# Performance work log

Measured on AMD Instinct MI355X. Metric: run time of the kernel, lower is better.

The kernel has to match this reference:

```python
import jax, jax.numpy as jnp
import numpy as np

VOCAB = 100000
EDIM = 300
MUS = np.array([-0.9, -0.7, -0.5, -0.3, -0.1, 0.1, 0.3, 0.5, 0.7, 0.9, 1.0], dtype=np.float32)
SIGMAS = np.array([0.1] * 10 + [0.001], dtype=np.float32)


def setup_inputs() -> dict:
    key = jax.random.key(0)
    k1, k2, k3, k4, k5, k6 = jax.random.split(key, 6)
    B, Q, D = 128, 16, 1024
    doctoks = jax.random.randint(k1, (B, D), 0, VOCAB)
    querytoks = jax.random.randint(k2, (B, Q), 0, VOCAB)
    query_idf = jax.random.uniform(k3, (B, Q), dtype=jnp.float32)
    emb_table = jax.random.normal(k4, (VOCAB, EDIM), dtype=jnp.float32) * 0.1
    # pad token 0 -> zero embedding (padding_idx semantics)
    emb_table = emb_table.at[0].set(0.0)
    mus = jnp.asarray(MUS)
    sigmas = jnp.asarray(SIGMAS)
    K = mus.shape[0]
    fc_w = jax.random.normal(k5, (1, K), dtype=jnp.float32) * (1.0 / np.sqrt(K))
    fc_b = jax.random.normal(k6, (1,), dtype=jnp.float32) * 0.01
    return {"doctoks": doctoks, "querytoks": querytoks, "query_idf": query_idf,
            "emb_table": emb_table, "mus": mus, "sigmas": sigmas,
            "fc_w": fc_w, "fc_b": fc_b}


def reference(doctoks, querytoks, query_idf, emb_table, mus, sigmas, fc_w, fc_b):
    eps = 1e-9
    q_emb = emb_table[querytoks]                # [B,Q,E]
    d_emb = emb_table[doctoks]                  # [B,D,E]
    qn = q_emb / (jnp.linalg.norm(q_emb, axis=-1, keepdims=True) + eps)
    dn = d_emb / (jnp.linalg.norm(d_emb, axis=-1, keepdims=True) + eps)
    simmat = jnp.einsum('bqe,bde->bqd', qn, dn)  # cosine sim [B,Q,D]
    # zero out padded positions (token id 0)
    pad_mask = (querytoks != 0)[:, :, None] & (doctoks != 0)[:, None, :]
    simmat = jnp.where(pad_mask, simmat, 0.0)
    # RBF kernel bank broadcast at dim=1: [B,K,Q,D]
    diff = simmat[:, None, :, :] - mus[None, :, None, None]
    kernels = jnp.exp(-0.5 * diff * diff / (sigmas[None, :, None, None] ** 2))
    result = kernels.sum(axis=3)                 # [B,K,Q]
    mask = (simmat.sum(axis=2) != 0.0)[:, None, :]  # [B,1,Q] -> broadcasts over K
    mask = jnp.broadcast_to(mask, result.shape)
    result = jnp.where(mask, jnp.log(result + 1e-6), 0.0)
    result = result.sum(axis=2)                  # [B,K]
    scores = result @ fc_w.T + fc_b              # [B,1]
    return scores
```

## Files before the change

kernel.cpp:

```cpp
#include <hip/hip_runtime.h>

#define EDIM 300
#define NB   128
#define NQ   16
#define ND   1024
#define NK   11
#define BLOCK 128
#define MDOC  4
#define TDOCS 256
#define BLOCKS_PER_B 4
#define NPANEL 10
#define PPITCH 36
#define SIMP 260

#define BARRIER_LGKM() do { \
    asm volatile("s_waitcnt lgkmcnt(0)" ::: "memory"); \
    __builtin_amdgcn_s_barrier(); \
    asm volatile("" ::: "memory"); } while (0)

#define PF_L(j)  pf##j = *(const float4*)(rp##j + pp * 32)
#define PF_LOAD(p) do { const int pp = (p); if (pp < 9 || s < 3) { \
    PF_L(0);  PF_L(1);  PF_L(2);  PF_L(3);  PF_L(4);  PF_L(5);  PF_L(6);  PF_L(7); \
    PF_L(8);  PF_L(9);  PF_L(10); PF_L(11); PF_L(12); PF_L(13); PF_L(14); PF_L(15); } } while (0)

#define PF_S(j)  *(float4*)&panel[(r0 + 16 * (j)) * PPITCH + s * 4] = pf##j
#define PF_WRITE(p) do { if ((p) < 9 || s < 3) { \
    PF_S(0);  PF_S(1);  PF_S(2);  PF_S(3);  PF_S(4);  PF_S(5);  PF_S(6);  PF_S(7); \
    PF_S(8);  PF_S(9);  PF_S(10); PF_S(11); PF_S(12); PF_S(13); PF_S(14); PF_S(15); } } while (0)

__global__ __launch_bounds__(BLOCK, 1) void knrm_main(
    const int*   __restrict__ dtoks,
    const int*   __restrict__ qtoks,
    const float* __restrict__ emb,
    const float* __restrict__ mus,
    const float* __restrict__ sigmas,
    float*       __restrict__ part) {
    __shared__ __align__(16) float qn_s[NQ * EDIM];
    __shared__ __align__(16) float panel[TDOCS * PPITCH];
    __shared__ int   dtok_s[TDOCS];
    __shared__ float rs_s[NQ];
    __shared__ __align__(16) float sim_t[NQ * SIMP];
    __shared__ float red_s[NK * NQ * 8];

    const int blk   = blockIdx.x;
    const int b     = blk >> 2;
    const int dbase = (blk & 3) * TDOCS;
    const int tid   = threadIdx.x;
    const int lane  = tid & 63;
    const int w     = tid >> 6;

    for (int i = tid; i < TDOCS; i += BLOCK) dtok_s[i] = dtoks[b * ND + dbase + i];
    for (int i = tid; i < NQ * (EDIM / 4); i += BLOCK) {
        int q = i / (EDIM / 4), e4 = i - q * (EDIM / 4);
        ((float4*)qn_s)[i] =
            *(const float4*)(emb + (size_t)qtoks[b * NQ + q] * EDIM + e4 * 4);
    }
    __syncthreads();

    const int s  = tid & 7;
    const int r0 = tid >> 3;

    const float* rp0  = emb + (size_t)dtok_s[r0 +   0] * EDIM + s * 4;
    const float* rp1  = emb + (size_t)dtok_s[r0 +  16] * EDIM + s * 4;
    const float* rp2  = emb + (size_t)dtok_s[r0 +  32] * EDIM + s * 4;
    const float* rp3  = emb + (size_t)dtok_s[r0 +  48] * EDIM + s * 4;
    const float* rp4  = emb + (size_t)dtok_s[r0 +  64] * EDIM + s * 4;
    const float* rp5  = emb + (size_t)dtok_s[r0 +  80] * EDIM + s * 4;
    const float* rp6  = emb + (size_t)dtok_s[r0 +  96] * EDIM + s * 4;
    const float* rp7  = emb + (size_t)dtok_s[r0 + 112] * EDIM + s * 4;
    const float* rp8  = emb + (size_t)dtok_s[r0 + 128] * EDIM + s * 4;
    const float* rp9  = emb + (size_t)dtok_s[r0 + 144] * EDIM + s * 4;
    const float* rp10 = emb + (size_t)dtok_s[r0 + 160] * EDIM + s * 4;
    const float* rp11 = emb + (size_t)dtok_s[r0 + 176] * EDIM + s * 4;
    const float* rp12 = emb + (size_t)dtok_s[r0 + 192] * EDIM + s * 4;
    const float* rp13 = emb + (size_t)dtok_s[r0 + 208] * EDIM + s * 4;
    const float* rp14 = emb + (size_t)dtok_s[r0 + 224] * EDIM + s * 4;
    const float* rp15 = emb + (size_t)dtok_s[r0 + 240] * EDIM + s * 4;

    float4 pf0, pf1, pf2, pf3, pf4, pf5, pf6, pf7,
           pf8, pf9, pf10, pf11, pf12, pf13, pf14, pf15;

    PF_LOAD(0);
    {
        int q = tid >> 3, j = tid & 7;
        float ss = 0.f;
        for (int e = j; e < EDIM; e += 8) { float v = qn_s[q * EDIM + e]; ss += v * v; }
        ss += __shfl_xor(ss, 1, 64);
        ss += __shfl_xor(ss, 2, 64);
        ss += __shfl_xor(ss, 4, 64);
        if (j == 0) rs_s[q] = 1.0f / (sqrtf(ss) + 1e-9f);
    }
    __syncthreads();
    for (int i = tid; i < NQ * (EDIM / 4); i += BLOCK) {
        float4 v = ((float4*)qn_s)[i];
        float r = rs_s[i / (EDIM / 4)];
        v.x *= r; v.y *= r; v.z *= r; v.w *= r;
        ((float4*)qn_s)[i] = v;
    }
    PF_WRITE(0);
    PF_LOAD(1);
    BARRIER_LGKM();

    float sims[MDOC][8];
#pragma unroll
    for (int m = 0; m < MDOC; ++m)
#pragma unroll
        for (int qq = 0; qq < 8; ++qq) sims[m][qq] = 0.f;
    float ssq[MDOC] = {0.f, 0.f, 0.f, 0.f};

    for (int p = 0; p < NPANEL; ++p) {
        const int cmax = (p == 9) ? 3 : 8;
        for (int cc = 0; cc < cmax; ++cc) {
            float4 dv[MDOC];
#pragma unroll
            for (int m = 0; m < MDOC; ++m)
                dv[m] = *(const float4*)&panel[(lane + 64 * m) * PPITCH + cc * 4];
#pragma unroll
            for (int m = 0; m < MDOC; ++m)
                ssq[m] += dv[m].x*dv[m].x + dv[m].y*dv[m].y + dv[m].z*dv[m].z + dv[m].w*dv[m].w;
            const float* qb = qn_s + (size_t)w * 8 * EDIM + (p * 8 + cc) * 4;
#pragma unroll
            for (int qq = 0; qq < 8; ++qq) {
                float4 qv = *(const float4*)(qb + qq * EDIM);
#pragma unroll
                for (int m = 0; m < MDOC; ++m) {
                    sims[m][qq] += qv.x*dv[m].x + qv.y*dv[m].y + qv.z*dv[m].z + qv.w*dv[m].w;
                }
            }
        }
        BARRIER_LGKM();
        if (p < 9) {
            PF_WRITE(p + 1);
            if (p < 8) PF_LOAD(p + 2);
            BARRIER_LGKM();
        }
    }

#pragma unroll
    for (int m = 0; m < MDOC; ++m) {
        float rn = 1.0f / (sqrtf(ssq[m]) + 1e-9f);
#pragma unroll
        for (int qq = 0; qq < 8; ++qq)
            sim_t[(w * 8 + qq) * SIMP + lane + 64 * m] = sims[m][qq] * rn;
    }
    __syncthreads();

    {
        const int q = tid & 15;
        const int sl = tid >> 4;
        float mu[NK], cc2[NK], acc[NK];
#pragma unroll
        for (int k = 0; k < NK; ++k) {
            mu[k] = mus[k];
            float sg = sigmas[k];
            cc2[k] = -0.5f / (sg * sg);
            acc[k] = 0.f;
        }
        const float* row = sim_t + q * SIMP + sl * 32;
#pragma unroll
        for (int i = 0; i < 8; ++i) {
            float4 s4 = *(const float4*)(row + i * 4);
#pragma unroll
            for (int k = 0; k < NK; ++k) {
                float e0 = s4.x - mu[k], e1 = s4.y - mu[k];
                float e2 = s4.z - mu[k], e3 = s4.w - mu[k];
                acc[k] += __expf(cc2[k]*e0*e0) + __expf(cc2[k]*e1*e1)
                        + __expf(cc2[k]*e2*e2) + __expf(cc2[k]*e3*e3);
            }
        }
#pragma unroll
        for (int k = 0; k < NK; ++k) red_s[(k * NQ + q) * 8 + sl] = acc[k];
    }
    __syncthreads();

    for (int t = tid; t < NK * NQ; t += BLOCK) {
        float r = 0.f;
#pragma unroll
        for (int j = 0; j < 8; ++j) r += red_s[t * 8 + j];
        part[blk * (NK * NQ) + t] = r;
    }
}

__global__ void knrm_final(const float* __restrict__ part,
                           const int*   __restrict__ qtoks,
                           const float* __restrict__ fc_w,
                           const float* __restrict__ fc_b,
                           float*       __restrict__ out) {
    __shared__ float red[NK * NQ];
    __shared__ float ks[NK];
    int b = blockIdx.x;
    int t = threadIdx.x;
    if (t < NK * NQ) {
        int q = t & 15;
        float r = 0.f;
        for (int j = 0; j < BLOCKS_PER_B; ++j)
            r += part[(b * BLOCKS_PER_B + j) * (NK * NQ) + t];
        red[t] = (qtoks[b * NQ + q] != 0) ? logf(r + 1e-6f) : 0.f;
    }
    __syncthreads();
    if (t < NK) {
        float s = 0.f;
        for (int q = 0; q < NQ; ++q) s += red[t * NQ + q];
        ks[t] = s * fc_w[t];
    }
    __syncthreads();
    if (t == 0) {
        float s = fc_b[0];
        for (int k = 0; k < NK; ++k) s += ks[k];
        out[b] = s;
    }
}

extern "C" void kernel_launch(void* const* d_in, const int* in_sizes, int n_in,
                              void* d_out, int out_size, void* d_ws, size_t ws_size,
                              hipStream_t stream) {
    const int*   doctoks   = (const int*)  d_in[0];
    const int*   querytoks = (const int*)  d_in[1];
    const float* emb       = (const float*)d_in[3];
    const float* mus       = (const float*)d_in[4];
    const float* sigmas    = (const float*)d_in[5];
    const float* fc_w      = (const float*)d_in[6];
    const float* fc_b      = (const float*)d_in[7];
    float* out = (float*)d_out;

    float* part = (float*)d_ws;

    knrm_main<<<NB * BLOCKS_PER_B, BLOCK, 0, stream>>>(doctoks, querytoks, emb,
                                                       mus, sigmas, part);
    knrm_final<<<NB, 192, 0, stream>>>(part, querytoks, fc_w, fc_b, out);
}
```

Measured before the change: 215.3 us.

## Double block threads to 256 and split work over query and doc halves

Raises the main kernel block size from 128 to 256 threads. Each wave now owns 8 queries and half of the documents (2 docs per lane instead of 4). The gather prefetch is redistributed over more threads, and the RBF reduction uses wave shuffles before a smaller shared-memory reduction. The aim is more waves per CU to hide gather latency and LDS stalls. The cost is that document norms are computed redundantly by two waves and each thread reads q vectors for fewer docs, which lowers register reuse.

```diff
diff --git a/kernel.cpp b/kernel.cpp
--- a/kernel.cpp
+++ b/kernel.cpp
@@ -5,8 +5,8 @@
 #define NQ   16
 #define ND   1024
 #define NK   11
-#define BLOCK 128
-#define MDOC  4
+#define BLOCK 256
+#define MDOC  2
 #define TDOCS 256
 #define BLOCKS_PER_B 4
 #define NPANEL 10
@@ -20,13 +20,11 @@
 
 #define PF_L(j)  pf##j = *(const float4*)(rp##j + pp * 32)
 #define PF_LOAD(p) do { const int pp = (p); if (pp < 9 || s < 3) { \
-    PF_L(0);  PF_L(1);  PF_L(2);  PF_L(3);  PF_L(4);  PF_L(5);  PF_L(6);  PF_L(7); \
-    PF_L(8);  PF_L(9);  PF_L(10); PF_L(11); PF_L(12); PF_L(13); PF_L(14); PF_L(15); } } while (0)
-
-#define PF_S(j)  *(float4*)&panel[(r0 + 16 * (j)) * PPITCH + s * 4] = pf##j
+    PF_L(0); PF_L(1); PF_L(2); PF_L(3); PF_L(4); PF_L(5); PF_L(6); PF_L(7); } } while (0)
+
+#define PF_S(j)  *(float4*)&panel[(r0 + 32 * (j)) * PPITCH + s * 4] = pf##j
 #define PF_WRITE(p) do { if ((p) < 9 || s < 3) { \
-    PF_S(0);  PF_S(1);  PF_S(2);  PF_S(3);  PF_S(4);  PF_S(5);  PF_S(6);  PF_S(7); \
-    PF_S(8);  PF_S(9);  PF_S(10); PF_S(11); PF_S(12); PF_S(13); PF_S(14); PF_S(15); } } while (0)
+    PF_S(0); PF_S(1); PF_S(2); PF_S(3); PF_S(4); PF_S(5); PF_S(6); PF_S(7); } } while (0)
 
 __global__ __launch_bounds__(BLOCK, 1) void knrm_main(
     const int*   __restrict__ dtoks,
@@ -40,7 +38,7 @@
     __shared__ int   dtok_s[TDOCS];
     __shared__ float rs_s[NQ];
     __shared__ __align__(16) float sim_t[NQ * SIMP];
-    __shared__ float red_s[NK * NQ * 8];
+    __shared__ float red_s[NK * NQ * 4];
 
     const int blk   = blockIdx.x;
     const int b     = blk >> 2;
@@ -48,6 +46,8 @@
     const int tid   = threadIdx.x;
     const int lane  = tid & 63;
     const int w     = tid >> 6;
+    const int qh    = w & 1;
+    const int dh    = w >> 1;
 
     for (int i = tid; i < TDOCS; i += BLOCK) dtok_s[i] = dtoks[b * ND + dbase + i];
     for (int i = tid; i < NQ * (EDIM / 4); i += BLOCK) {
@@ -60,34 +60,26 @@
     const int s  = tid & 7;
     const int r0 = tid >> 3;
 
-    const float* rp0  = emb + (size_t)dtok_s[r0 +   0] * EDIM + s * 4;
-    const float* rp1  = emb + (size_t)dtok_s[r0 +  16] * EDIM + s * 4;
-    const float* rp2  = emb + (size_t)dtok_s[r0 +  32] * EDIM + s * 4;
-    const float* rp3  = emb + (size_t)dtok_s[r0 +  48] * EDIM + s * 4;
-    const float* rp4  = emb + (size_t)dtok_s[r0 +  64] * EDIM + s * 4;
-    const float* rp5  = emb + (size_t)dtok_s[r0 +  80] * EDIM + s * 4;
-    const float* rp6  = emb + (size_t)dtok_s[r0 +  96] * EDIM + s * 4;
-    const float* rp7  = emb + (size_t)dtok_s[r0 + 112] * EDIM + s * 4;
-    const float* rp8  = emb + (size_t)dtok_s[r0 + 128] * EDIM + s * 4;
-    const float* rp9  = emb + (size_t)dtok_s[r0 + 144] * EDIM + s * 4;
-    const float* rp10 = emb + (size_t)dtok_s[r0 + 160] * EDIM + s * 4;
-    const float* rp11 = emb + (size_t)dtok_s[r0 + 176] * EDIM + s * 4;
-    const float* rp12 = emb + (size_t)dtok_s[r0 + 192] * EDIM + s * 4;
-    const float* rp13 = emb + (size_t)dtok_s[r0 + 208] * EDIM + s * 4;
-    const float* rp14 = emb + (size_t)dtok_s[r0 + 224] * EDIM + s * 4;
-    const float* rp15 = emb + (size_t)dtok_s[r0 + 240] * EDIM + s * 4;
-
-    float4 pf0, pf1, pf2, pf3, pf4, pf5, pf6, pf7,
-           pf8, pf9, pf10, pf11, pf12, pf13, pf14, pf15;
+    const float* rp0 = emb + (size_t)dtok_s[r0 +   0] * EDIM + s * 4;
+    const float* rp1 = emb + (size_t)dtok_s[r0 +  32] * EDIM + s * 4;
+    const float* rp2 = emb + (size_t)dtok_s[r0 +  64] * EDIM + s * 4;
+    const float* rp3 = emb + (size_t)dtok_s[r0 +  96] * EDIM + s * 4;
+    const float* rp4 = emb + (size_t)dtok_s[r0 + 128] * EDIM + s * 4;
+    const float* rp5 = emb + (size_t)dtok_s[r0 + 160] * EDIM + s * 4;
+    const float* rp6 = emb + (size_t)dtok_s[r0 + 192] * EDIM + s * 4;
+    const float* rp7 = emb + (size_t)dtok_s[r0 + 224] * EDIM + s * 4;
+
+    float4 pf0, pf1, pf2, pf3, pf4, pf5, pf6, pf7;
 
     PF_LOAD(0);
     {
-        int q = tid >> 3, j = tid & 7;
+        int q = tid >> 4, j = tid & 15;
         float ss = 0.f;
-        for (int e = j; e < EDIM; e += 8) { float v = qn_s[q * EDIM + e]; ss += v * v; }
+        for (int e = j; e < EDIM; e += 16) { float v = qn_s[q * EDIM + e]; ss += v * v; }
         ss += __shfl_xor(ss, 1, 64);
         ss += __shfl_xor(ss, 2, 64);
         ss += __shfl_xor(ss, 4, 64);
+        ss += __shfl_xor(ss, 8, 64);
         if (j == 0) rs_s[q] = 1.0f / (sqrtf(ss) + 1e-9f);
     }
     __syncthreads();
@@ -106,7 +98,9 @@
     for (int m = 0; m < MDOC; ++m)
 #pragma unroll
         for (int qq = 0; qq < 8; ++qq) sims[m][qq] = 0.f;
-    float ssq[MDOC] = {0.f, 0.f, 0.f, 0.f};
+    float ssq[MDOC] = {0.f, 0.f};
+
+    const float* qbase = qn_s + (size_t)qh * 8 * EDIM;
 
     for (int p = 0; p < NPANEL; ++p) {
         const int cmax = (p == 9) ? 3 : 8;
@@ -114,11 +108,11 @@
             float4 dv[MDOC];
 #pragma unroll
             for (int m = 0; m < MDOC; ++m)
-                dv[m] = *(const float4*)&panel[(lane + 64 * m) * PPITCH + cc * 4];
+                dv[m] = *(const float4*)&panel[(lane + 64 * (m + 2 * dh)) * PPITCH + cc * 4];
 #pragma unroll
             for (int m = 0; m < MDOC; ++m)
                 ssq[m] += dv[m].x*dv[m].x + dv[m].y*dv[m].y + dv[m].z*dv[m].z + dv[m].w*dv[m].w;
-            const float* qb = qn_s + (size_t)w * 8 * EDIM + (p * 8 + cc) * 4;
+            const float* qb = qbase + (p * 8 + cc) * 4;
 #pragma unroll
             for (int qq = 0; qq < 8; ++qq) {
                 float4 qv = *(const float4*)(qb + qq * EDIM);
@@ -141,12 +135,12 @@
         float rn = 1.0f / (sqrtf(ssq[m]) + 1e-9f);
 #pragma unroll
         for (int qq = 0; qq < 8; ++qq)
-            sim_t[(w * 8 + qq) * SIMP + lane + 64 * m] = sims[m][qq] * rn;
+            sim_t[(qh * 8 + qq) * SIMP + lane + 64 * m + 128 * dh] = sims[m][qq] * rn;
     }
     __syncthreads();
 
     {
-        const int q = tid & 15;
+        const int q  = tid & 15;
         const int sl = tid >> 4;
         float mu[NK], cc2[NK], acc[NK];
 #pragma unroll
@@ -156,9 +150,9 @@
             cc2[k] = -0.5f / (sg * sg);
             acc[k] = 0.f;
         }
-        const float* row = sim_t + q * SIMP + sl * 32;
-#pragma unroll
-        for (int i = 0; i < 8; ++i) {
+        const float* row = sim_t + q * SIMP + sl * 16;
+#pragma unroll
+        for (int i = 0; i < 4; ++i) {
             float4 s4 = *(const float4*)(row + i * 4);
 #pragma unroll
             for (int k = 0; k < NK; ++k) {
@@ -169,14 +163,20 @@
             }
         }
 #pragma unroll
-        for (int k = 0; k < NK; ++k) red_s[(k * NQ + q) * 8 + sl] = acc[k];
+        for (int k = 0; k < NK; ++k) {
+            acc[k] += __shfl_xor(acc[k], 16, 64);
+            acc[k] += __shfl_xor(acc[k], 32, 64);
+        }
+        if ((sl & 3) == 0) {
+#pragma unroll
+            for (int k = 0; k < NK; ++k)
+                red_s[(k * NQ + q) * 4 + (sl >> 2)] = acc[k];
+        }
     }
     __syncthreads();
 
     for (int t = tid; t < NK * NQ; t += BLOCK) {
-        float r = 0.f;
-#pragma unroll
-        for (int j = 0; j < 8; ++j) r += red_s[t * 8 + j];
+        float r = red_s[t * 4] + red_s[t * 4 + 1] + red_s[t * 4 + 2] + red_s[t * 4 + 3];
         part[blk * (NK * NQ) + t] = r;
     }
 }
```

Result: no change. 212.3 us (-1.4%).
